# Optimization experiments

Measured on AMD Instinct MI355X. Metric: run time of the kernel, lower is better.

Reference implementation:

```python
import jax, jax.numpy as jnp
import numpy as np

T, N, U, K, P = 4096, 256, 128, 32, 128


def setup_inputs() -> dict:
    key = jax.random.key(0)
    ks = jax.random.split(key, 8)
    input_sequence = jax.random.normal(ks[0], (T, U, K), jnp.float32)
    # Stable diagonal dynamics: |A| in (0.5, 0.99), random phase.
    r = jax.random.uniform(ks[1], (N, K), jnp.float32, 0.5, 0.99)
    theta = jax.random.uniform(ks[2], (N, K), jnp.float32, 0.0, np.pi)
    A_re = r * jnp.cos(theta)
    A_im = r * jnp.sin(theta)
    s_b = 1.0 / np.sqrt(U)
    s_c = 1.0 / np.sqrt(N)
    B_re = jax.random.normal(ks[3], (N, U), jnp.float32) * s_b
    B_im = jax.random.normal(ks[4], (N, U), jnp.float32) * s_b
    C_re = jax.random.normal(ks[5], (P, N), jnp.float32) * s_c
    C_im = jax.random.normal(ks[6], (P, N), jnp.float32) * s_c
    D = jax.random.normal(ks[7], (P, U), jnp.float32) * s_b
    return dict(input_sequence=input_sequence, A_re=A_re, A_im=A_im,
                B_re=B_re, B_im=B_im, C_re=C_re, C_im=C_im, D=D)


def _binary_op(elem_i, elem_j):
    # (a_i, s_i) o (a_j, s_j) = (a_i * a_j, a_j * s_i + s_j)
    a_i, s_i = elem_i
    a_j, s_j = elem_j
    return (a_i * a_j, a_j * s_i + s_j)


def reference(input_sequence, A_re, A_im, B_re, B_im, C_re, C_im, D):
    A = (A_re + 1j * A_im).astype(jnp.complex64)        # (N, K) diagonal
    Bm = (B_re + 1j * B_im).astype(jnp.complex64)        # (N, U)
    Cm = (C_re + 1j * C_im).astype(jnp.complex64)        # (P, N)
    x_c = input_sequence.astype(jnp.complex64)           # (T, U, K)
    # inputs_t = B @ x_t  -> (T, N, K)
    inputs = jnp.einsum('nu,tuk->tnk', Bm, x_c)
    systems = jnp.broadcast_to(A, (input_sequence.shape[0],) + A.shape)
    _, states = jax.lax.associative_scan(_binary_op, (systems, inputs))
    # out_t = C @ state_t -> (T, P, K)
    out = jnp.real(jnp.einsum('pn,tnk->tpk', Cm, states))
    Du = jnp.einsum('pu,tuk->tpk', D, input_sequence)    # 2D D branch
    return out + Du
```

## Files before the change

### kernel.cpp

```cpp
#include <hip/hip_runtime.h>
#include <hip/hip_bf16.h>

namespace {

constexpr int T = 4096, N = 256, U = 128, K = 32, P = 128;
constexpr int NK = N * K;
constexpr int CL = 16;
constexpr int NCH = T / CL;
constexpr int NG = NCH / 8;
constexpr int TB = 8;

typedef __attribute__((ext_vector_type(8))) short short8;
typedef __attribute__((ext_vector_type(4))) float f32x4;
typedef __attribute__((address_space(3))) unsigned lds_u32;
typedef __attribute__((address_space(1))) const unsigned glb_u32;

__device__ __forceinline__ unsigned short f2bf(float f) {
  union { float f; unsigned u; } v; v.f = f;
  unsigned r = v.u + 0x7FFFu + ((v.u >> 16) & 1u);
  return (unsigned short)(r >> 16);
}
__device__ __forceinline__ float bf2f(unsigned short s) {
  union { unsigned u; float f; } v; v.u = ((unsigned)s) << 16;
  return v.f;
}
__device__ __forceinline__ short8 ld8(const unsigned short* p) {
  return *reinterpret_cast<const short8*>(p);
}
__device__ __forceinline__ void dma16(const unsigned* g, unsigned* l) {
  __builtin_amdgcn_global_load_lds((glb_u32*)g, (lds_u32*)l, 16, 0, 0);
}
__device__ __forceinline__ void csq(float& pr, float& pi) {
  float nr = pr * pr - pi * pi, ni = 2.f * pr * pi; pr = nr; pi = ni;
}

__device__ __forceinline__ int zswz(int k, int n) {
  int n8 = n >> 3, j = n & 7;
  return k * 256 + ((n8 ^ (k & 7)) << 3) + (j ^ (((k >> 3) & 1) << 2));
}

__device__ __forceinline__ void unpackAB(uint4 a, uint4 b, short8& re, short8& im) {
  union { short8 v; unsigned u[4]; } r, i;
  r.u[0] = (a.x & 0xFFFFu) | (a.y << 16);
  i.u[0] = (a.x >> 16)     | (a.y & 0xFFFF0000u);
  r.u[1] = (a.z & 0xFFFFu) | (a.w << 16);
  i.u[1] = (a.z >> 16)     | (a.w & 0xFFFF0000u);
  r.u[2] = (b.x & 0xFFFFu) | (b.y << 16);
  i.u[2] = (b.x >> 16)     | (b.y & 0xFFFF0000u);
  r.u[3] = (b.z & 0xFFFFu) | (b.w << 16);
  i.u[3] = (b.z >> 16)     | (b.w & 0xFFFF0000u);
  re = r.v; im = i.v;
}

__global__ __launch_bounds__(256) void k_params(
    const float* Are, const float* Aim, const float* Bre, const float* Bim,
    const float* Cre, const float* Cim, const float* D,
    unsigned short* bre, unsigned short* bim, unsigned short* cre,
    unsigned short* cimn, unsigned short* dbf, float* atre, float* atim) {
  int idx = blockIdx.x * 256 + threadIdx.x;
  int stride = gridDim.x * 256;
  for (int i = idx; i < N * U; i += stride) { bre[i] = f2bf(Bre[i]); bim[i] = f2bf(Bim[i]); }
  for (int i = idx; i < P * N; i += stride) { cre[i] = f2bf(Cre[i]); cimn[i] = f2bf(-Cim[i]); }
  for (int i = idx; i < P * U; i += stride) { dbf[i] = f2bf(D[i]); }
  for (int i = idx; i < NK; i += stride) {
    int k = i >> 8, r = i & 255;
    int n8 = (r >> 3) ^ (k & 7);
    int j  = (r & 7) ^ (((k >> 3) & 1) << 2);
    int n = n8 * 8 + j;
    atre[i] = Are[n * K + k];
    atim[i] = Aim[n * K + k];
  }
}

__global__ __launch_bounds__(256) void k_castx(const float* x, unsigned* xTu) {
  __shared__ float lds[U * 33];
  int t = blockIdx.x, tid = threadIdx.x;
  const float* xt = x + (size_t)t * (U * K);
#pragma unroll
  for (int it = 0; it < 16; it++) {
    int idx = it * 256 + tid;
    int u = idx >> 5, k = idx & 31;
    lds[u * 33 + k] = xt[idx];
  }
  __syncthreads();
  unsigned* dst = xTu + (size_t)t * (K * U / 2);
#pragma unroll
  for (int it = 0; it < 8; it++) {
    int k = it * 4 + (tid >> 6);
    int up = tid & 63;
    float f0 = lds[(2 * up) * 33 + k];
    float f1 = lds[(2 * up + 1) * 33 + k];
    dst[k * 64 + up] = (unsigned)f2bf(f0) | ((unsigned)f2bf(f1) << 16);
  }
}

__global__ __launch_bounds__(256)
__attribute__((amdgpu_waves_per_eu(2, 2)))
void k_bgemm(const unsigned short* xT, const unsigned short* bre,
             const unsigned short* bim, unsigned* zbuf, int t0) {
  int blk = blockIdx.x, tid = threadIdx.x;
  int w = tid >> 6, l = tid & 63, lq = l >> 4, lr = l & 15;
  short8 Bf_re[4][4], Bf_im[4][4];
#pragma unroll
  for (int s = 0; s < 4; s++)
#pragma unroll
    for (int nt = 0; nt < 4; nt++) {
      int n0 = (w * 4 + nt) * 16;
      Bf_re[s][nt] = ld8(bre + (n0 + lr) * U + s * 32 + lq * 8);
      Bf_im[s][nt] = ld8(bim + (n0 + lr) * U + s * 32 + lq * 8);
    }
#pragma unroll
  for (int tl = 0; tl < TB; tl++) {
    int tloc = blk * TB + tl;
    const unsigned short* xrow = xT + (size_t)(t0 + tloc) * (K * U);
    short8 af[4][2];
#pragma unroll
    for (int s = 0; s < 4; s++) {
      af[s][0] = ld8(xrow + lr * U + s * 32 + lq * 8);
      af[s][1] = ld8(xrow + (16 + lr) * U + s * 32 + lq * 8);
    }
    f32x4 accre[2][4], accim[2][4];
#pragma unroll
    for (int a = 0; a < 2; a++)
#pragma unroll
      for (int b = 0; b < 4; b++) { accre[a][b] = (f32x4)0.f; accim[a][b] = (f32x4)0.f; }
#pragma unroll
    for (int s = 0; s < 4; s++)
#pragma unroll
      for (int nt = 0; nt < 4; nt++)
#pragma unroll
        for (int mt = 0; mt < 2; mt++) {
          accre[mt][nt] = __builtin_amdgcn_mfma_f32_16x16x32_bf16(af[s][mt], Bf_re[s][nt], accre[mt][nt], 0, 0, 0);
          accim[mt][nt] = __builtin_amdgcn_mfma_f32_16x16x32_bf16(af[s][mt], Bf_im[s][nt], accim[mt][nt], 0, 0, 0);
        }
    unsigned* dst = zbuf + (size_t)tloc * NK;
#pragma unroll
    for (int mt = 0; mt < 2; mt++)
#pragma unroll
      for (int nt = 0; nt < 4; nt++) {
        int n0 = (w * 4 + nt) * 16;
#pragma unroll
        for (int r = 0; r < 4; r++) {
          int krow = mt * 16 + lq * 4 + r;
          dst[zswz(krow, n0 + lr)] =
              (unsigned)f2bf(accre[mt][nt][r]) | ((unsigned)f2bf(accim[mt][nt][r]) << 16);
        }
      }
  }
}

__global__ __launch_bounds__(256) void k_scanA(const unsigned* zbuf, const float* atre,
                                               const float* atim, float2* cend, int c0) {
  int bid = blockIdx.x;
  int cl = bid >> 5;
  int lane = (bid & 31) * 256 + threadIdx.x;
  float ar = atre[lane], ai = atim[lane];
  float sr = 0.f, si = 0.f;
  const unsigned* src = zbuf + (size_t)cl * CL * NK + lane;
#pragma unroll 8
  for (int i = 0; i < CL; i++) {
    unsigned v = src[(size_t)i * NK];
    float ur = bf2f((unsigned short)(v & 0xFFFFu));
    float ui = bf2f((unsigned short)(v >> 16));
    float nr = ar * sr - ai * si + ur;
    float ni = ar * si + ai * sr + ui;
    sr = nr; si = ni;
  }
  cend[(size_t)(c0 + cl) * NK + lane] = make_float2(sr, si);
}

__global__ __launch_bounds__(256) void k_carryg(const float2* cend, const float* atre,
                                                const float* atim, float2* gagg) {
  int bid = blockIdx.x;
  int g = bid >> 5;
  int lane = (bid & 31) * 256 + threadIdx.x;
  float pr = atre[lane], pi = atim[lane];
#pragma unroll
  for (int i = 0; i < 4; i++) csq(pr, pi);
  float agr = 0.f, agi = 0.f;
#pragma unroll
  for (int j = 0; j < 8; j++) {
    float2 e = cend[(size_t)(g * 8 + j) * NK + lane];
    float nr = pr * agr - pi * agi + e.x;
    float ni = pr * agi + pi * agr + e.y;
    agr = nr; agi = ni;
  }
  gagg[(size_t)g * NK + lane] = make_float2(agr, agi);
}

__global__ __launch_bounds__(256) void k_carryb(float2* gagg, const float* atre,
                                                const float* atim) {
  int lane = blockIdx.x * 256 + threadIdx.x;
  float pr = atre[lane], pi = atim[lane];
#pragma unroll
  for (int i = 0; i < 7; i++) csq(pr, pi);
  float cr = 0.f, ci = 0.f;
  for (int gg = 0; gg < NG / 8; gg++) {
    float2 buf[8];
#pragma unroll
    for (int j = 0; j < 8; j++) buf[j] = gagg[(size_t)(gg * 8 + j) * NK + lane];
#pragma unroll
    for (int j = 0; j < 8; j++) {
      gagg[(size_t)(gg * 8 + j) * NK + lane] = make_float2(cr, ci);
      float nr = pr * cr - pi * ci + buf[j].x;
      float ni = pr * ci + pi * cr + buf[j].y;
      cr = nr; ci = ni;
    }
  }
}

__global__ __launch_bounds__(256) void k_carryf(float2* cend, const float* atre,
                                                const float* atim, const float2* gagg) {
  int bid = blockIdx.x;
  int g = bid >> 5;
  int lane = (bid & 31) * 256 + threadIdx.x;
  float pr = atre[lane], pi = atim[lane];
#pragma unroll
  for (int i = 0; i < 4; i++) csq(pr, pi);
  float2 c = gagg[(size_t)g * NK + lane];
  float cr = c.x, ci = c.y;
#pragma unroll
  for (int j = 0; j < 8; j++) {
    size_t off = (size_t)(g * 8 + j) * NK + lane;
    float2 e = cend[off];
    cend[off] = make_float2(cr, ci);
    float nr = pr * cr - pi * ci + e.x;
    float ni = pr * ci + pi * cr + e.y;
    cr = nr; ci = ni;
  }
}

__global__ __launch_bounds__(512)
__attribute__((amdgpu_waves_per_eu(2, 2)))
void k_scout(const unsigned* zbuf, const float* atre, const float* atim,
             const float2* cend,
             const unsigned short* cre, const unsigned short* cimn,
             const unsigned short* dbf, const unsigned short* xT,
             float* out, int t0, int gc0) {
  __shared__ unsigned ldsz[2][NK];
  int blk = blockIdx.x, tid = threadIdx.x;
  int w = tid >> 6, l = tid & 63, lq = l >> 4, lr = l & 15;
  int h = (lr >> 3) & 1;
  short8 Cf_re[8], Cf_im[8];
#pragma unroll
  for (int s = 0; s < 8; s++) {
    int p = w * 16 + lr;
    Cf_re[s] = ld8(cre  + p * N + s * 32 + lq * 8);
    Cf_im[s] = ld8(cimn + p * N + s * 32 + lq * 8);
  }
  short8 Df[4];
#pragma unroll
  for (int s = 0; s < 4; s++) {
    int p = w * 16 + lr;
    Df[s] = ld8(dbf + p * U + s * 32 + lq * 8);
  }
  float ar[16], ai[16], sr[16], si[16];
  int gc = gc0 + blk;
#pragma unroll
  for (int it = 0; it < 4; it++)
#pragma unroll
    for (int j = 0; j < 4; j++) {
      int idx = it * 2048 + tid * 4 + j;
      int e = it * 4 + j;
      ar[e] = atre[idx]; ai[e] = atim[idx];
      float2 c0 = cend[(size_t)gc * NK + idx];
      sr[e] = c0.x; si[e] = c0.y;
    }
  {
    const unsigned* z0 = zbuf + (size_t)(blk * CL) * NK;
#pragma unroll
    for (int it = 0; it < 4; it++)
      dma16(z0 + it * 2048 + tid * 4, &ldsz[0][it * 2048 + tid * 4]);
  }
  __syncthreads();
  int cur = 0;
  for (int tl = 0; tl < CL; tl++) {
    int tloc = blk * CL + tl;
    int t = t0 + tloc;
    if (tl + 1 < CL) {
      const unsigned* zn = zbuf + (size_t)(tloc + 1) * NK;
#pragma unroll
      for (int it = 0; it < 4; it++)
        dma16(zn + it * 2048 + tid * 4, &ldsz[cur ^ 1][it * 2048 + tid * 4]);
    }
    const unsigned short* xt = xT + (size_t)t * (K * U);
    short8 xfr[4][2];
#pragma unroll
    for (int s = 0; s < 4; s++)
#pragma unroll
      for (int kt = 0; kt < 2; kt++)
        xfr[s][kt] = ld8(xt + (kt * 16 + lr) * U + s * 32 + lq * 8);
    unsigned* zl = &ldsz[cur][0];
#pragma unroll
    for (int it = 0; it < 4; it++) {
      unsigned* p4 = zl + it * 2048 + tid * 4;
      uint4 v = *reinterpret_cast<const uint4*>(p4);
      unsigned d0 = v.x, d1 = v.y, d2 = v.z, d3 = v.w;
#pragma unroll
      for (int j = 0; j < 4; j++) {
        unsigned dv = (j == 0) ? d0 : (j == 1) ? d1 : (j == 2) ? d2 : d3;
        int e = it * 4 + j;
        float ur = bf2f((unsigned short)(dv & 0xFFFFu));
        float ui = bf2f((unsigned short)(dv >> 16));
        float nr = ar[e] * sr[e] - ai[e] * si[e] + ur;
        float ni = ar[e] * si[e] + ai[e] * sr[e] + ui;
        sr[e] = nr; si[e] = ni;
        dv = (unsigned)f2bf(nr) | ((unsigned)f2bf(ni) << 16);
        if (j == 0) d0 = dv; else if (j == 1) d1 = dv; else if (j == 2) d2 = dv; else d3 = dv;
      }
      uint4 o; o.x = d0; o.y = d1; o.z = d2; o.w = d3;
      *reinterpret_cast<uint4*>(p4) = o;
    }
    __syncthreads();
    f32x4 acc[2];
    acc[0] = (f32x4)0.f; acc[1] = (f32x4)0.f;
    const unsigned* zs = &ldsz[cur][0];
#pragma unroll
    for (int s = 0; s < 8; s++) {
      short8 bfr[2], bfi[2];
#pragma unroll
      for (int kt = 0; kt < 2; kt++) {
        int k = kt * 16 + lr;
        int n8 = s * 4 + lq;
        const uint4* qp = reinterpret_cast<const uint4*>(zs + k * 256 + ((n8 ^ (k & 7)) << 3));
        uint4 a = qp[h], b = qp[h ^ 1];
        unpackAB(a, b, bfr[kt], bfi[kt]);
      }
#pragma unroll
      for (int kt = 0; kt < 2; kt++) {
        acc[kt] = __builtin_amdgcn_mfma_f32_16x16x32_bf16(Cf_re[s], bfr[kt], acc[kt], 0, 0, 0);
        acc[kt] = __builtin_amdgcn_mfma_f32_16x16x32_bf16(Cf_im[s], bfi[kt], acc[kt], 0, 0, 0);
      }
    }
#pragma unroll
    for (int s = 0; s < 4; s++)
#pragma unroll
      for (int kt = 0; kt < 2; kt++)
        acc[kt] = __builtin_amdgcn_mfma_f32_16x16x32_bf16(Df[s], xfr[s][kt], acc[kt], 0, 0, 0);
    float* ot = out + (size_t)t * (P * K);
#pragma unroll
    for (int kt = 0; kt < 2; kt++)
#pragma unroll
      for (int r = 0; r < 4; r++) {
        int p = w * 16 + lq * 4 + r;
        int k = kt * 16 + lr;
        ot[p * K + k] = acc[kt][r];
      }
    __syncthreads();
    cur ^= 1;
  }
}

}

extern "C" void kernel_launch(void* const* d_in, const int* in_sizes, int n_in,
                              void* d_out, int out_size, void* d_ws, size_t ws_size,
                              hipStream_t stream) {
  const float* x   = (const float*)d_in[0];
  const float* Are = (const float*)d_in[1];
  const float* Aim = (const float*)d_in[2];
  const float* Bre = (const float*)d_in[3];
  const float* Bim = (const float*)d_in[4];
  const float* Cre = (const float*)d_in[5];
  const float* Cim = (const float*)d_in[6];
  const float* D   = (const float*)d_in[7];
  float* out = (float*)d_out;

  auto al = [](size_t x_) { return (x_ + 255) & ~(size_t)255; };
  const size_t fixed = al((size_t)T * K * U * 2)
                     + al((size_t)NCH * NK * 8)
                     + al((size_t)NG * NK * 8)
                     + 2 * al((size_t)N * U * 2)
                     + 2 * al((size_t)P * N * 2)
                     + al((size_t)P * U * 2)
                     + 2 * al((size_t)NK * 4);
  int S = 64;
  for (int s : {1, 2, 4, 8, 16, 32, 64}) {
    if (fixed + al((size_t)(T / s) * NK * 4) <= ws_size) { S = s; break; }
  }
  const int TS = T / S;
  const int CS = NCH / S;

  char* w = (char*)d_ws;
  auto alloc = [&](size_t bytes) { void* p = (void*)w; w += (bytes + 255) & ~(size_t)255; return p; };
  unsigned* zbuf       = (unsigned*)alloc((size_t)TS * NK * 4);
  unsigned* xTu        = (unsigned*)alloc((size_t)T * K * U * 2);
  float2* cend         = (float2*)alloc((size_t)NCH * NK * 8);
  float2* gagg         = (float2*)alloc((size_t)NG * NK * 8);
  unsigned short* bre  = (unsigned short*)alloc((size_t)N * U * 2);
  unsigned short* bim  = (unsigned short*)alloc((size_t)N * U * 2);
  unsigned short* cre  = (unsigned short*)alloc((size_t)P * N * 2);
  unsigned short* cimn = (unsigned short*)alloc((size_t)P * N * 2);
  unsigned short* dbf  = (unsigned short*)alloc((size_t)P * U * 2);
  float* atre          = (float*)alloc((size_t)NK * 4);
  float* atim          = (float*)alloc((size_t)NK * 4);

  k_params<<<64, 256, 0, stream>>>(Are, Aim, Bre, Bim, Cre, Cim, D,
                                   bre, bim, cre, cimn, dbf, atre, atim);
  k_castx<<<T, 256, 0, stream>>>(x, xTu);

  const unsigned short* xT16 = (const unsigned short*)xTu;
  for (int q = 0; q < S; q++) {
    k_bgemm<<<TS / TB, 256, 0, stream>>>(xT16, bre, bim, zbuf, q * TS);
    k_scanA<<<CS * 32, 256, 0, stream>>>(zbuf, atre, atim, cend, q * CS);
  }
  k_carryg<<<NG * 32, 256, 0, stream>>>(cend, atre, atim, gagg);
  k_carryb<<<NK / 256, 256, 0, stream>>>(gagg, atre, atim);
  k_carryf<<<NG * 32, 256, 0, stream>>>(cend, atre, atim, gagg);
  for (int q = 0; q < S; q++) {
    if (S > 1)
      k_bgemm<<<TS / TB, 256, 0, stream>>>(xT16, bre, bim, zbuf, q * TS);
    k_scout<<<TS / CL, 512, 0, stream>>>(zbuf, atre, atim, cend,
                                         cre, cimn, dbf, xT16, out, q * TS, q * CS);
  }
}
```

Measured before the change: 269.1 us.

## Split scan-output kernel across K halves to double block count

```diff
diff --git a/kernel.cpp b/kernel.cpp
--- a/kernel.cpp
+++ b/kernel.cpp
@@ -9,6 +9,7 @@
 constexpr int NCH = T / CL;
 constexpr int NG = NCH / 8;
 constexpr int TB = 8;
+constexpr int HK = NK / 2;
 
 typedef __attribute__((ext_vector_type(8))) short short8;
 typedef __attribute__((ext_vector_type(4))) float f32x4;
@@ -230,15 +231,15 @@
   }
 }
 
-__global__ __launch_bounds__(512)
-__attribute__((amdgpu_waves_per_eu(2, 2)))
+__global__ __launch_bounds__(512, 4)
 void k_scout(const unsigned* zbuf, const float* atre, const float* atim,
              const float2* cend,
              const unsigned short* cre, const unsigned short* cimn,
              const unsigned short* dbf, const unsigned short* xT,
              float* out, int t0, int gc0) {
-  __shared__ unsigned ldsz[2][NK];
+  __shared__ unsigned ldsz[2][HK];
   int blk = blockIdx.x, tid = threadIdx.x;
+  int ch = blk >> 1, kh = blk & 1;
   int w = tid >> 6, l = tid & 63, lq = l >> 4, lr = l & 15;
   int h = (lr >> 3) & 1;
   short8 Cf_re[8], Cf_im[8];
@@ -254,45 +255,43 @@
     int p = w * 16 + lr;
     Df[s] = ld8(dbf + p * U + s * 32 + lq * 8);
   }
-  float ar[16], ai[16], sr[16], si[16];
-  int gc = gc0 + blk;
-#pragma unroll
-  for (int it = 0; it < 4; it++)
+  float ar[8], ai[8], sr[8], si[8];
+  int gc = gc0 + ch;
+#pragma unroll
+  for (int it = 0; it < 2; it++)
 #pragma unroll
     for (int j = 0; j < 4; j++) {
-      int idx = it * 2048 + tid * 4 + j;
+      int idx = kh * HK + it * 2048 + tid * 4 + j;
       int e = it * 4 + j;
       ar[e] = atre[idx]; ai[e] = atim[idx];
       float2 c0 = cend[(size_t)gc * NK + idx];
       sr[e] = c0.x; si[e] = c0.y;
     }
   {
-    const unsigned* z0 = zbuf + (size_t)(blk * CL) * NK;
-#pragma unroll
-    for (int it = 0; it < 4; it++)
+    const unsigned* z0 = zbuf + (size_t)(ch * CL) * NK + kh * HK;
+#pragma unroll
+    for (int it = 0; it < 2; it++)
       dma16(z0 + it * 2048 + tid * 4, &ldsz[0][it * 2048 + tid * 4]);
   }
   __syncthreads();
   int cur = 0;
   for (int tl = 0; tl < CL; tl++) {
-    int tloc = blk * CL + tl;
+    int tloc = ch * CL + tl;
     int t = t0 + tloc;
     if (tl + 1 < CL) {
-      const unsigned* zn = zbuf + (size_t)(tloc + 1) * NK;
-#pragma unroll
-      for (int it = 0; it < 4; it++)
+      const unsigned* zn = zbuf + (size_t)(tloc + 1) * NK + kh * HK;
+#pragma unroll
+      for (int it = 0; it < 2; it++)
         dma16(zn + it * 2048 + tid * 4, &ldsz[cur ^ 1][it * 2048 + tid * 4]);
     }
     const unsigned short* xt = xT + (size_t)t * (K * U);
-    short8 xfr[4][2];
+    short8 xfr[4];
 #pragma unroll
     for (int s = 0; s < 4; s++)
-#pragma unroll
-      for (int kt = 0; kt < 2; kt++)
-        xfr[s][kt] = ld8(xt + (kt * 16 + lr) * U + s * 32 + lq * 8);
+      xfr[s] = ld8(xt + (kh * 16 + lr) * U + s * 32 + lq * 8);
     unsigned* zl = &ldsz[cur][0];
 #pragma unroll
-    for (int it = 0; it < 4; it++) {
+    for (int it = 0; it < 2; it++) {
       unsigned* p4 = zl + it * 2048 + tid * 4;
       uint4 v = *reinterpret_cast<const uint4*>(p4);
       unsigned d0 = v.x, d1 = v.y, d2 = v.z, d3 = v.w;
@@ -312,40 +311,27 @@
       *reinterpret_cast<uint4*>(p4) = o;
     }
     __syncthreads();
-    f32x4 acc[2];
-    acc[0] = (f32x4)0.f; acc[1] = (f32x4)0.f;
+    f32x4 acc = (f32x4)0.f;
     const unsigned* zs = &ldsz[cur][0];
 #pragma unroll
     for (int s = 0; s < 8; s++) {
-      short8 bfr[2], bfi[2];
-#pragma unroll
-      for (int kt = 0; kt < 2; kt++) {
-        int k = kt * 16 + lr;
-        int n8 = s * 4 + lq;
-        const uint4* qp = reinterpret_cast<const uint4*>(zs + k * 256 + ((n8 ^ (k & 7)) << 3));
-        uint4 a = qp[h], b = qp[h ^ 1];
-        unpackAB(a, b, bfr[kt], bfi[kt]);
-      }
-#pragma unroll
-      for (int kt = 0; kt < 2; kt++) {
-        acc[kt] = __builtin_amdgcn_mfma_f32_16x16x32_bf16(Cf_re[s], bfr[kt], acc[kt], 0, 0, 0);
-        acc[kt] = __builtin_amdgcn_mfma_f32_16x16x32_bf16(Cf_im[s], bfi[kt], acc[kt], 0, 0, 0);
-      }
+      short8 bfr, bfi;
+      int n8 = s * 4 + lq;
+      const uint4* qp = reinterpret_cast<const uint4*>(zs + lr * 256 + ((n8 ^ (lr & 7)) << 3));
+      uint4 a = qp[h], b = qp[h ^ 1];
+      unpackAB(a, b, bfr, bfi);
+      acc = __builtin_amdgcn_mfma_f32_16x16x32_bf16(Cf_re[s], bfr, acc, 0, 0, 0);
+      acc = __builtin_amdgcn_mfma_f32_16x16x32_bf16(Cf_im[s], bfi, acc, 0, 0, 0);
     }
 #pragma unroll
     for (int s = 0; s < 4; s++)
-#pragma unroll
-      for (int kt = 0; kt < 2; kt++)
-        acc[kt] = __builtin_amdgcn_mfma_f32_16x16x32_bf16(Df[s], xfr[s][kt], acc[kt], 0, 0, 0);
+      acc = __builtin_amdgcn_mfma_f32_16x16x32_bf16(Df[s], xfr[s], acc, 0, 0, 0);
     float* ot = out + (size_t)t * (P * K);
 #pragma unroll
-    for (int kt = 0; kt < 2; kt++)
-#pragma unroll
-      for (int r = 0; r < 4; r++) {
-        int p = w * 16 + lq * 4 + r;
-        int k = kt * 16 + lr;
-        ot[p * K + k] = acc[kt][r];
-      }
+    for (int r = 0; r < 4; r++) {
+      int p = w * 16 + lq * 4 + r;
+      ot[p * K + kh * 16 + lr] = acc[r];
+    }
     __syncthreads();
     cur ^= 1;
   }
@@ -410,7 +396,7 @@
   for (int q = 0; q < S; q++) {
     if (S > 1)
       k_bgemm<<<TS / TB, 256, 0, stream>>>(xT16, bre, bim, zbuf, q * TS);
-    k_scout<<<TS / CL, 512, 0, stream>>>(zbuf, atre, atim, cend,
-                                         cre, cimn, dbf, xT16, out, q * TS, q * CS);
-  }
-}
+    k_scout<<<(TS / CL) * 2, 512, 0, stream>>>(zbuf, atre, atim, cend,
+                                               cre, cimn, dbf, xT16, out, q * TS, q * CS);
+  }
+}
```

After: 361.1 us. 1.34x slower.

## Triple-buffer LDS z tiles with prefetch distance two and explicit waitcnts

Applied to the files above, without the earlier changes.

```diff
diff --git a/kernel.cpp b/kernel.cpp
--- a/kernel.cpp
+++ b/kernel.cpp
@@ -237,7 +237,7 @@
              const unsigned short* cre, const unsigned short* cimn,
              const unsigned short* dbf, const unsigned short* xT,
              float* out, int t0, int gc0) {
-  __shared__ unsigned ldsz[2][NK];
+  __shared__ unsigned ldsz[3][NK];
   int blk = blockIdx.x, tid = threadIdx.x;
   int w = tid >> 6, l = tid & 63, lq = l >> 4, lr = l & 15;
   int h = (lr >> 3) & 1;
@@ -266,23 +266,17 @@
       float2 c0 = cend[(size_t)gc * NK + idx];
       sr[e] = c0.x; si[e] = c0.y;
     }
-  {
-    const unsigned* z0 = zbuf + (size_t)(blk * CL) * NK;
-#pragma unroll
-    for (int it = 0; it < 4; it++)
-      dma16(z0 + it * 2048 + tid * 4, &ldsz[0][it * 2048 + tid * 4]);
-  }
-  __syncthreads();
-  int cur = 0;
+  const unsigned* zch = zbuf + (size_t)(blk * CL) * NK;
+#pragma unroll
+  for (int it = 0; it < 4; it++)
+    dma16(zch + it * 2048 + tid * 4, &ldsz[0][it * 2048 + tid * 4]);
+#pragma unroll
+  for (int it = 0; it < 4; it++)
+    dma16(zch + NK + it * 2048 + tid * 4, &ldsz[1][it * 2048 + tid * 4]);
+
+  int bc = 0;
   for (int tl = 0; tl < CL; tl++) {
-    int tloc = blk * CL + tl;
-    int t = t0 + tloc;
-    if (tl + 1 < CL) {
-      const unsigned* zn = zbuf + (size_t)(tloc + 1) * NK;
-#pragma unroll
-      for (int it = 0; it < 4; it++)
-        dma16(zn + it * 2048 + tid * 4, &ldsz[cur ^ 1][it * 2048 + tid * 4]);
-    }
+    int t = t0 + blk * CL + tl;
     const unsigned short* xt = xT + (size_t)t * (K * U);
     short8 xfr[4][2];
 #pragma unroll
@@ -290,7 +284,9 @@
 #pragma unroll
       for (int kt = 0; kt < 2; kt++)
         xfr[s][kt] = ld8(xt + (kt * 16 + lr) * U + s * 32 + lq * 8);
-    unsigned* zl = &ldsz[cur][0];
+    if (tl == 0) { asm volatile("s_waitcnt vmcnt(12)" ::: "memory"); }
+    else         { asm volatile("s_waitcnt vmcnt(20)" ::: "memory"); }
+    unsigned* zl = &ldsz[bc][0];
 #pragma unroll
     for (int it = 0; it < 4; it++) {
       unsigned* p4 = zl + it * 2048 + tid * 4;
@@ -311,10 +307,19 @@
       uint4 o; o.x = d0; o.y = d1; o.z = d2; o.w = d3;
       *reinterpret_cast<uint4*>(p4) = o;
     }
-    __syncthreads();
+    asm volatile("s_waitcnt lgkmcnt(0)" ::: "memory");
+    __builtin_amdgcn_s_barrier();
+    __builtin_amdgcn_sched_barrier(0);
+    if (tl + 2 < CL) {
+      int bn = bc + 2; if (bn >= 3) bn -= 3;
+      const unsigned* zn = zbuf + (size_t)(blk * CL + tl + 2) * NK;
+#pragma unroll
+      for (int it = 0; it < 4; it++)
+        dma16(zn + it * 2048 + tid * 4, &ldsz[bn][it * 2048 + tid * 4]);
+    }
     f32x4 acc[2];
     acc[0] = (f32x4)0.f; acc[1] = (f32x4)0.f;
-    const unsigned* zs = &ldsz[cur][0];
+    const unsigned* zs = &ldsz[bc][0];
 #pragma unroll
     for (int s = 0; s < 8; s++) {
       short8 bfr[2], bfi[2];
@@ -346,8 +351,7 @@
         int k = kt * 16 + lr;
         ot[p * K + k] = acc[kt][r];
       }
-    __syncthreads();
-    cur ^= 1;
+    bc = bc + 1; if (bc >= 3) bc -= 3;
   }
 }
 
```

Measured after the change: 265.8 us. Within noise of the previous version (-1.2%).
